# Kernel tuning notes

Hardware: AMD Instinct MI355X
Metric: run time of the kernel (lower is better)

The kernel has to match this reference:

```python
import jax, jax.numpy as jnp
import numpy as np

COMPRESSION = 2  # max-pool factor along flattened spatial axis for phi and g


def setup_inputs() -> dict:
    key = jax.random.key(0)
    ks = jax.random.split(key, 5)
    B, C, H, W = 4, 64, 96, 96
    Ci = 32  # intermediate_dim = C // 2
    s = 1.0 / np.sqrt(C)
    return {
        "x": jax.random.normal(ks[0], (B, C, H, W), dtype=jnp.float32),
        "w_theta": jax.random.normal(ks[1], (Ci, C), dtype=jnp.float32) * s,
        "b_theta": jnp.zeros((Ci,), dtype=jnp.float32),
        "w_phi": jax.random.normal(ks[2], (Ci, C), dtype=jnp.float32) * s,
        "b_phi": jnp.zeros((Ci,), dtype=jnp.float32),
        "w_g": jax.random.normal(ks[3], (Ci, C), dtype=jnp.float32) * s,
        "b_g": jnp.zeros((Ci,), dtype=jnp.float32),
        "w_out": jax.random.normal(ks[4], (C, Ci), dtype=jnp.float32) * (1.0 / np.sqrt(Ci)),
        "b_out": jnp.zeros((C,), dtype=jnp.float32),
    }


def reference(x, w_theta, b_theta, w_phi, b_phi, w_g, b_g, w_out, b_out):
    B, C, H, W = x.shape
    N = H * W
    xf = x.reshape(B, C, N).transpose(0, 2, 1)            # [B, N, C]
    # 1x1 conv projections == channel matmuls
    theta = xf @ w_theta.T + b_theta                      # [B, N, Ci]
    phi = xf @ w_phi.T + b_phi                            # [B, N, Ci]
    g = xf @ w_g.T + b_g                                  # [B, N, Ci]
    # compression: max-pool (kernel=stride=COMPRESSION) along flattened spatial axis
    Ci = theta.shape[-1]
    phi = phi.reshape(B, N // COMPRESSION, COMPRESSION, Ci).max(axis=2)  # [B, N/c, Ci]
    g = g.reshape(B, N // COMPRESSION, COMPRESSION, Ci).max(axis=2)      # [B, N/c, Ci]
    # embedded-gaussian affinity + softmax
    attn = jax.nn.softmax(jnp.einsum('bnc,bmc->bnm', theta, phi), axis=-1)  # [B, N, N/c]
    y = jnp.einsum('bnm,bmc->bnc', attn, g)               # [B, N, Ci]
    out = y @ w_out.T + b_out                             # [B, N, C]
    out = out.transpose(0, 2, 1).reshape(B, C, H, W)
    return out + x  # residual
```

## Files before the change

### kernel.cpp

```cpp
#include <hip/hip_runtime.h>
#include <hip/hip_bf16.h>


#define NQ 9216
#define MM 4608
#define TPW 36
#define LOG2E 1.44269504088896340736f

typedef __attribute__((ext_vector_type(8))) short bf16x8;
typedef __attribute__((ext_vector_type(4))) float f32x4;
typedef __attribute__((ext_vector_type(4))) unsigned short u16x4;

static __device__ __forceinline__ unsigned pk2(float a, float b) {
    __hip_bfloat162 h = __float22bfloat162_rn(make_float2(a, b));
    return *reinterpret_cast<unsigned*>(&h);
}

__global__ __launch_bounds__(128, 4) void proj_kernel(
    const float* __restrict__ x,
    const float* __restrict__ wt, const float* __restrict__ bt,
    const float* __restrict__ wp, const float* __restrict__ bp,
    const float* __restrict__ wg, const float* __restrict__ bg,
    unsigned short* __restrict__ theta, unsigned short* __restrict__ phi,
    unsigned short* __restrict__ gT)
{
    __shared__ unsigned short gst[32 * 20];

    const int tid  = threadIdx.x;
    const int wid  = tid >> 6;
    const int lane = tid & 63;
    const int q = lane >> 4;
    const int c = lane & 15;

    const int b     = blockIdx.x / 288;
    const int rem   = blockIdx.x % 288;
    const int n0    = rem * 32 + wid * 16;

    const float* Wm[3] = {wt, wp, wg};
    const float* Bm[3] = {bt, bp, bg};

    bf16x8 wf[3][2][2];
    float bias[3][2];
#pragma unroll
    for (int p = 0; p < 3; ++p) {
#pragma unroll
        for (int ct = 0; ct < 2; ++ct) {
            bias[p][ct] = Bm[p][ct * 16 + c];
#pragma unroll
            for (int ks = 0; ks < 2; ++ks) {
                const float* wsrc = Wm[p] + (ct * 16 + c) * 64 + ks * 32 + q * 8;
                f32x4 w0 = *(const f32x4*)wsrc;
                f32x4 w1 = *(const f32x4*)(wsrc + 4);
                unsigned* wk = (unsigned*)&wf[p][ct][ks];
                wk[0] = pk2(w0[0], w0[1]); wk[1] = pk2(w0[2], w0[3]);
                wk[2] = pk2(w1[0], w1[1]); wk[3] = pk2(w1[2], w1[3]);
            }
        }
    }

    bf16x8 af[2];
#pragma unroll
    for (int ks = 0; ks < 2; ++ks) {
        unsigned* ap = (unsigned*)&af[ks];
#pragma unroll
        for (int j2 = 0; j2 < 4; ++j2) {
            float x0 = x[(b * 64 + ks * 32 + q * 8 + j2 * 2) * NQ + n0 + c];
            float x1 = x[(b * 64 + ks * 32 + q * 8 + j2 * 2 + 1) * NQ + n0 + c];
            ap[j2] = pk2(x0, x1);
        }
    }

#pragma unroll
    for (int p = 0; p < 3; ++p) {
#pragma unroll
        for (int ct = 0; ct < 2; ++ct) {
            f32x4 acc = {0.f, 0.f, 0.f, 0.f};
            acc = __builtin_amdgcn_mfma_f32_16x16x32_bf16(af[0], wf[p][ct][0], acc, 0, 0, 0);
            acc = __builtin_amdgcn_mfma_f32_16x16x32_bf16(af[1], wf[p][ct][1], acc, 0, 0, 0);
#pragma unroll
            for (int r = 0; r < 4; ++r) acc[r] += bias[p][ct];
            const int ci = ct * 16 + c;
            if (p == 0) {
                unsigned pv0 = pk2(acc[0] * LOG2E, acc[1] * LOG2E);
                unsigned pv1 = pk2(acc[2] * LOG2E, acc[3] * LOG2E);
                theta[(b * NQ + n0 + 4 * q + 0) * 32 + ci] = (unsigned short)pv0;
                theta[(b * NQ + n0 + 4 * q + 1) * 32 + ci] = (unsigned short)(pv0 >> 16);
                theta[(b * NQ + n0 + 4 * q + 2) * 32 + ci] = (unsigned short)pv1;
                theta[(b * NQ + n0 + 4 * q + 3) * 32 + ci] = (unsigned short)(pv1 >> 16);
            } else {
                unsigned pv = pk2(fmaxf(acc[0], acc[1]), fmaxf(acc[2], acc[3]));
                if (p == 1) {
                    const int m0 = (n0 >> 1) + 2 * q;
                    phi[(b * MM + m0) * 32 + ci]     = (unsigned short)pv;
                    phi[(b * MM + m0 + 1) * 32 + ci] = (unsigned short)(pv >> 16);
                } else {
                    *(unsigned int*)(gst + ci * 20 + wid * 8 + 2 * q) = pv;
                }
            }
        }
    }

    __syncthreads();
    {
        const int ci = tid >> 2;
        const int m4 = (tid & 3) * 4;
        u16x4 v = *(const u16x4*)(gst + ci * 20 + m4);
        *(u16x4*)(gT + (b * 32 + ci) * MM + rem * 16 + m4) = v;
    }
}

__global__ __launch_bounds__(256, 4) void attn_kernel(
    const unsigned short* __restrict__ theta, const unsigned short* __restrict__ phi,
    const unsigned short* __restrict__ gT,
    const float* __restrict__ w_out, const float* __restrict__ b_out,
    const float* __restrict__ x, float* __restrict__ out)
{
    __shared__ union SharedU {
        unsigned short pld[4][48 * 32];
        struct {
            float red[4][48][36];
            float lred[4][48];
            unsigned short yld[32][50];
        } ep;
    } sh;

    const int tid  = threadIdx.x;
    const int w    = tid >> 6;
    const int lane = tid & 63;
    const int q  = lane >> 4;
    const int c  = lane & 15;
    const int sw = ((c >> 1) & 3) << 3;

    const int b  = blockIdx.x / 192;
    const int nb = (blockIdx.x % 192) * 48;

    bf16x8 qf[3];
#pragma unroll
    for (int rt = 0; rt < 3; ++rt)
        qf[rt] = *(const bf16x8*)(theta + (b * NQ + nb + rt * 16 + c) * 32 + q * 8);

    const unsigned short* phiB = phi + (size_t)b * MM * 32;
    const unsigned short* gTB  = gT + (size_t)b * 32 * MM;
    unsigned short* myp = sh.pld[w];

    f32x4 acc[3][2];
    float lsum[3];
#pragma unroll
    for (int rt = 0; rt < 3; ++rt) {
        lsum[rt] = 0.f;
#pragma unroll
        for (int s2 = 0; s2 < 2; ++s2) acc[rt][s2] = (f32x4){0.f, 0.f, 0.f, 0.f};
    }

    const int t0 = w * TPW;
    bf16x8 kf[2], vf[2];

#define LOAD_KF(m0) do {                                                      \
    kf[0] = *(const bf16x8*)(phiB + ((m0) + c) * 32 + q * 8);                 \
    kf[1] = *(const bf16x8*)(phiB + ((m0) + 16 + c) * 32 + q * 8);            \
} while (0)

#define LOAD_VF(m0) do {                                                      \
    vf[0] = *(const bf16x8*)(gTB + c * MM + (m0) + q * 8);                    \
    vf[1] = *(const bf16x8*)(gTB + (16 + c) * MM + (m0) + q * 8);             \
} while (0)

#define S_STEP(rt) do {                                                      \
    _Pragma("unroll")                                                        \
    for (int mct = 0; mct < 2; ++mct) {                                      \
        f32x4 z = {0.f, 0.f, 0.f, 0.f};                                      \
        f32x4 s = __builtin_amdgcn_mfma_f32_16x16x32_bf16(kf[mct], qf[rt], z, 0, 0, 0); \
        float e0 = __builtin_amdgcn_exp2f(s[0]);                             \
        float e1 = __builtin_amdgcn_exp2f(s[1]);                             \
        float e2 = __builtin_amdgcn_exp2f(s[2]);                             \
        float e3 = __builtin_amdgcn_exp2f(s[3]);                             \
        lsum[rt] += (e0 + e1) + (e2 + e3);                                   \
        uint2 hv = {pk2(e0, e1), pk2(e2, e3)};                               \
        *(uint2*)(myp + (((rt) * 16 + c) << 5) + ((mct * 16 + 4 * q) ^ sw)) = hv; \
    }                                                                        \
} while (0)

#define PV_STEP(rt) do {                                                     \
    bf16x8 pf = *(const bf16x8*)(myp + (((rt) * 16 + c) << 5) + ((q * 8) ^ sw)); \
    acc[rt][0] = __builtin_amdgcn_mfma_f32_16x16x32_bf16(vf[0], pf, acc[rt][0], 0, 0, 0); \
    acc[rt][1] = __builtin_amdgcn_mfma_f32_16x16x32_bf16(vf[1], pf, acc[rt][1], 0, 0, 0); \
} while (0)

    LOAD_KF(t0 * 32);
    LOAD_VF(t0 * 32);
    S_STEP(0); S_STEP(1); S_STEP(2);

    for (int mi = 1; mi < TPW; ++mi) {
        const int m0 = (t0 + mi) * 32;
        LOAD_KF(m0);
        PV_STEP(0); PV_STEP(1); PV_STEP(2);
        LOAD_VF(m0);
        S_STEP(0); S_STEP(1); S_STEP(2);
    }

    PV_STEP(0); PV_STEP(1); PV_STEP(2);

#undef LOAD_KF
#undef LOAD_VF
#undef S_STEP
#undef PV_STEP

    float lv[3];
#pragma unroll
    for (int rt = 0; rt < 3; ++rt) {
        float v = lsum[rt];
        v += __shfl_xor(v, 16);
        v += __shfl_xor(v, 32);
        lv[rt] = v;
    }

    __syncthreads();

    if (lane < 16) {
        sh.ep.lred[w][lane]      = lv[0];
        sh.ep.lred[w][16 + lane] = lv[1];
        sh.ep.lred[w][32 + lane] = lv[2];
    }
#pragma unroll
    for (int rt = 0; rt < 3; ++rt)
#pragma unroll
        for (int s2 = 0; s2 < 2; ++s2)
            *(f32x4*)&sh.ep.red[w][rt * 16 + c][s2 * 16 + 4 * q] = acc[rt][s2];

    __syncthreads();

    if (tid < 192) {
        const int n   = tid % 48;
        const int cig = (tid / 48) * 8;
        float ls = (sh.ep.lred[0][n] + sh.ep.lred[1][n]) +
                   (sh.ep.lred[2][n] + sh.ep.lred[3][n]);
        float inv = 1.0f / ls;
        f32x4 s0 = {0.f, 0.f, 0.f, 0.f}, s1 = {0.f, 0.f, 0.f, 0.f};
#pragma unroll
        for (int ww = 0; ww < 4; ++ww) {
            s0 += *(const f32x4*)&sh.ep.red[ww][n][cig];
            s1 += *(const f32x4*)&sh.ep.red[ww][n][cig + 4];
        }
#pragma unroll
        for (int k = 0; k < 4; ++k) {
            sh.ep.yld[cig + k][n]     = (unsigned short)(pk2(s0[k] * inv, 0.f) & 0xffff);
            sh.ep.yld[cig + 4 + k][n] = (unsigned short)(pk2(s1[k] * inv, 0.f) & 0xffff);
        }
    }
    __syncthreads();

    {
        bf16x8 wof;
        {
            const float* wsrc = w_out + (w * 16 + c) * 32 + q * 8;
            f32x4 w0 = *(const f32x4*)wsrc;
            f32x4 w1 = *(const f32x4*)(wsrc + 4);
            unsigned* wk = (unsigned*)&wof;
            wk[0] = pk2(w0[0], w0[1]); wk[1] = pk2(w0[2], w0[3]);
            wk[2] = pk2(w1[0], w1[1]); wk[3] = pk2(w1[2], w1[3]);
        }
#pragma unroll
        for (int nt = 0; nt < 3; ++nt) {
            bf16x8 yf;
            unsigned short* yp = (unsigned short*)&yf;
#pragma unroll
            for (int j = 0; j < 8; ++j)
                yp[j] = sh.ep.yld[q * 8 + j][nt * 16 + c];
            f32x4 z = {0.f, 0.f, 0.f, 0.f};
            f32x4 o = __builtin_amdgcn_mfma_f32_16x16x32_bf16(wof, yf, z, 0, 0, 0);
#pragma unroll
            for (int r = 0; r < 4; ++r) {
                const int chn = w * 16 + 4 * q + r;
                const size_t addr = (size_t)(b * 64 + chn) * NQ + nb + nt * 16 + c;
                out[addr] = o[r] + b_out[chn] + x[addr];
            }
        }
    }
}

extern "C" void kernel_launch(void* const* d_in, const int* in_sizes, int n_in,
                              void* d_out, int out_size, void* d_ws, size_t ws_size,
                              hipStream_t stream) {
    const float* x       = (const float*)d_in[0];
    const float* w_theta = (const float*)d_in[1];
    const float* b_theta = (const float*)d_in[2];
    const float* w_phi   = (const float*)d_in[3];
    const float* b_phi   = (const float*)d_in[4];
    const float* w_g     = (const float*)d_in[5];
    const float* b_g     = (const float*)d_in[6];
    const float* w_out   = (const float*)d_in[7];
    const float* b_out   = (const float*)d_in[8];
    float* out = (float*)d_out;

    unsigned short* theta = (unsigned short*)d_ws;
    unsigned short* phi   = theta + 4 * NQ * 32;
    unsigned short* gT    = phi + 4 * MM * 32;

    proj_kernel<<<1152, 128, 0, stream>>>(x, w_theta, b_theta, w_phi, b_phi,
                                          w_g, b_g, theta, phi, gT);
    attn_kernel<<<768, 256, 0, stream>>>(theta, phi, gT, w_out, b_out, x, out);
}
```

Measured before the change: 129.4 us.

## Compute softmax row sums with an MFMA and double proj work per block

The attention kernel no longer accumulates the softmax denominator with scalar adds and cross-lane shuffles. It runs an extra MFMA per PV step against a ones-vector operand, so the row sums come out of the matrix unit and take the bf16-rounded probabilities as input. This moves VALU work onto the matrix pipe but adds one MFMA for every two existing ones. Separately, the projection kernel now handles 64 spatial positions per block instead of 32, halving the grid and amortizing the weight loads and conversion, with a larger shared staging tile for the transposed g.

```diff
diff --git a/kernel.cpp b/kernel.cpp
--- a/kernel.cpp
+++ b/kernel.cpp
@@ -24,7 +24,7 @@
     unsigned short* __restrict__ theta, unsigned short* __restrict__ phi,
     unsigned short* __restrict__ gT)
 {
-    __shared__ unsigned short gst[32 * 20];
+    __shared__ unsigned short gst[32 * 36];
 
     const int tid  = threadIdx.x;
     const int wid  = tid >> 6;
@@ -32,9 +32,9 @@
     const int q = lane >> 4;
     const int c = lane & 15;
 
-    const int b     = blockIdx.x / 288;
-    const int rem   = blockIdx.x % 288;
-    const int n0    = rem * 32 + wid * 16;
+    const int b   = blockIdx.x / 144;
+    const int rem = blockIdx.x % 144;
+    const int n0  = rem * 64 + wid * 32;
 
     const float* Wm[3] = {wt, wp, wg};
     const float* Bm[3] = {bt, bp, bg};
@@ -58,43 +58,48 @@
         }
     }
 
-    bf16x8 af[2];
-#pragma unroll
-    for (int ks = 0; ks < 2; ++ks) {
-        unsigned* ap = (unsigned*)&af[ks];
-#pragma unroll
-        for (int j2 = 0; j2 < 4; ++j2) {
-            float x0 = x[(b * 64 + ks * 32 + q * 8 + j2 * 2) * NQ + n0 + c];
-            float x1 = x[(b * 64 + ks * 32 + q * 8 + j2 * 2 + 1) * NQ + n0 + c];
-            ap[j2] = pk2(x0, x1);
-        }
-    }
-
-#pragma unroll
-    for (int p = 0; p < 3; ++p) {
-#pragma unroll
-        for (int ct = 0; ct < 2; ++ct) {
-            f32x4 acc = {0.f, 0.f, 0.f, 0.f};
-            acc = __builtin_amdgcn_mfma_f32_16x16x32_bf16(af[0], wf[p][ct][0], acc, 0, 0, 0);
-            acc = __builtin_amdgcn_mfma_f32_16x16x32_bf16(af[1], wf[p][ct][1], acc, 0, 0, 0);
-#pragma unroll
-            for (int r = 0; r < 4; ++r) acc[r] += bias[p][ct];
-            const int ci = ct * 16 + c;
-            if (p == 0) {
-                unsigned pv0 = pk2(acc[0] * LOG2E, acc[1] * LOG2E);
-                unsigned pv1 = pk2(acc[2] * LOG2E, acc[3] * LOG2E);
-                theta[(b * NQ + n0 + 4 * q + 0) * 32 + ci] = (unsigned short)pv0;
-                theta[(b * NQ + n0 + 4 * q + 1) * 32 + ci] = (unsigned short)(pv0 >> 16);
-                theta[(b * NQ + n0 + 4 * q + 2) * 32 + ci] = (unsigned short)pv1;
-                theta[(b * NQ + n0 + 4 * q + 3) * 32 + ci] = (unsigned short)(pv1 >> 16);
-            } else {
-                unsigned pv = pk2(fmaxf(acc[0], acc[1]), fmaxf(acc[2], acc[3]));
-                if (p == 1) {
-                    const int m0 = (n0 >> 1) + 2 * q;
-                    phi[(b * MM + m0) * 32 + ci]     = (unsigned short)pv;
-                    phi[(b * MM + m0 + 1) * 32 + ci] = (unsigned short)(pv >> 16);
+#pragma unroll
+    for (int nt = 0; nt < 2; ++nt) {
+        const int n0t = n0 + nt * 16;
+
+        bf16x8 af[2];
+#pragma unroll
+        for (int ks = 0; ks < 2; ++ks) {
+            unsigned* ap = (unsigned*)&af[ks];
+#pragma unroll
+            for (int j2 = 0; j2 < 4; ++j2) {
+                float x0 = x[(b * 64 + ks * 32 + q * 8 + j2 * 2) * NQ + n0t + c];
+                float x1 = x[(b * 64 + ks * 32 + q * 8 + j2 * 2 + 1) * NQ + n0t + c];
+                ap[j2] = pk2(x0, x1);
+            }
+        }
+
+#pragma unroll
+        for (int p = 0; p < 3; ++p) {
+#pragma unroll
+            for (int ct = 0; ct < 2; ++ct) {
+                f32x4 acc = {0.f, 0.f, 0.f, 0.f};
+                acc = __builtin_amdgcn_mfma_f32_16x16x32_bf16(af[0], wf[p][ct][0], acc, 0, 0, 0);
+                acc = __builtin_amdgcn_mfma_f32_16x16x32_bf16(af[1], wf[p][ct][1], acc, 0, 0, 0);
+#pragma unroll
+                for (int r = 0; r < 4; ++r) acc[r] += bias[p][ct];
+                const int ci = ct * 16 + c;
+                if (p == 0) {
+                    unsigned pv0 = pk2(acc[0] * LOG2E, acc[1] * LOG2E);
+                    unsigned pv1 = pk2(acc[2] * LOG2E, acc[3] * LOG2E);
+                    theta[(b * NQ + n0t + 4 * q + 0) * 32 + ci] = (unsigned short)pv0;
+                    theta[(b * NQ + n0t + 4 * q + 1) * 32 + ci] = (unsigned short)(pv0 >> 16);
+                    theta[(b * NQ + n0t + 4 * q + 2) * 32 + ci] = (unsigned short)pv1;
+                    theta[(b * NQ + n0t + 4 * q + 3) * 32 + ci] = (unsigned short)(pv1 >> 16);
                 } else {
-                    *(unsigned int*)(gst + ci * 20 + wid * 8 + 2 * q) = pv;
+                    unsigned pv = pk2(fmaxf(acc[0], acc[1]), fmaxf(acc[2], acc[3]));
+                    if (p == 1) {
+                        const int m0 = (n0t >> 1) + 2 * q;
+                        phi[(b * MM + m0) * 32 + ci]     = (unsigned short)pv;
+                        phi[(b * MM + m0 + 1) * 32 + ci] = (unsigned short)(pv >> 16);
+                    } else {
+                        *(unsigned int*)(gst + ci * 36 + wid * 16 + nt * 8 + 2 * q) = pv;
+                    }
                 }
             }
         }
@@ -103,9 +108,12 @@
     __syncthreads();
     {
         const int ci = tid >> 2;
-        const int m4 = (tid & 3) * 4;
-        u16x4 v = *(const u16x4*)(gst + ci * 20 + m4);
-        *(u16x4*)(gT + (b * 32 + ci) * MM + rem * 16 + m4) = v;
+        const int m8 = (tid & 3) * 8;
+        u16x4 v0 = *(const u16x4*)(gst + ci * 36 + m8);
+        u16x4 v1 = *(const u16x4*)(gst + ci * 36 + m8 + 4);
+        unsigned short* dst = gT + (size_t)(b * 32 + ci) * MM + rem * 32 + m8;
+        *(u16x4*)dst       = v0;
+        *(u16x4*)(dst + 4) = v1;
     }
 }
 
@@ -139,15 +147,22 @@
     for (int rt = 0; rt < 3; ++rt)
         qf[rt] = *(const bf16x8*)(theta + (b * NQ + nb + rt * 16 + c) * 32 + q * 8);
 
+    bf16x8 onef;
+    {
+        unsigned v = (c == 0) ? 0x3F803F80u : 0u;
+        unsigned* op = (unsigned*)&onef;
+        op[0] = v; op[1] = v; op[2] = v; op[3] = v;
+    }
+
     const unsigned short* phiB = phi + (size_t)b * MM * 32;
     const unsigned short* gTB  = gT + (size_t)b * 32 * MM;
     unsigned short* myp = sh.pld[w];
 
     f32x4 acc[3][2];
-    float lsum[3];
+    f32x4 lacc[3];
 #pragma unroll
     for (int rt = 0; rt < 3; ++rt) {
-        lsum[rt] = 0.f;
+        lacc[rt] = (f32x4){0.f, 0.f, 0.f, 0.f};
 #pragma unroll
         for (int s2 = 0; s2 < 2; ++s2) acc[rt][s2] = (f32x4){0.f, 0.f, 0.f, 0.f};
     }
@@ -170,13 +185,9 @@
     for (int mct = 0; mct < 2; ++mct) {                                      \
         f32x4 z = {0.f, 0.f, 0.f, 0.f};                                      \
         f32x4 s = __builtin_amdgcn_mfma_f32_16x16x32_bf16(kf[mct], qf[rt], z, 0, 0, 0); \
-        float e0 = __builtin_amdgcn_exp2f(s[0]);                             \
-        float e1 = __builtin_amdgcn_exp2f(s[1]);                             \
-        float e2 = __builtin_amdgcn_exp2f(s[2]);                             \
-        float e3 = __builtin_amdgcn_exp2f(s[3]);                             \
-        lsum[rt] += (e0 + e1) + (e2 + e3);                                   \
-        uint2 hv = {pk2(e0, e1), pk2(e2, e3)};                               \
-        *(uint2*)(myp + (((rt) * 16 + c) << 5) + ((mct * 16 + 4 * q) ^ sw)) = hv; \
+        uint2 hv = {pk2(__builtin_amdgcn_exp2f(s[0]), __builtin_amdgcn_exp2f(s[1])),    \
+                    pk2(__builtin_amdgcn_exp2f(s[2]), __builtin_amdgcn_exp2f(s[3]))};   \
+        *(uint2*)(myp + (((rt) * 16 + c) << 5) + ((mct * 16 + 4 * q) ^ sw)) = hv;       \
     }                                                                        \
 } while (0)
 
@@ -184,6 +195,7 @@
     bf16x8 pf = *(const bf16x8*)(myp + (((rt) * 16 + c) << 5) + ((q * 8) ^ sw)); \
     acc[rt][0] = __builtin_amdgcn_mfma_f32_16x16x32_bf16(vf[0], pf, acc[rt][0], 0, 0, 0); \
     acc[rt][1] = __builtin_amdgcn_mfma_f32_16x16x32_bf16(vf[1], pf, acc[rt][1], 0, 0, 0); \
+    lacc[rt]   = __builtin_amdgcn_mfma_f32_16x16x32_bf16(onef,  pf, lacc[rt],   0, 0, 0); \
 } while (0)
 
     LOAD_KF(t0 * 32);
@@ -205,21 +217,12 @@
 #undef S_STEP
 #undef PV_STEP
 
-    float lv[3];
-#pragma unroll
-    for (int rt = 0; rt < 3; ++rt) {
-        float v = lsum[rt];
-        v += __shfl_xor(v, 16);
-        v += __shfl_xor(v, 32);
-        lv[rt] = v;
-    }
-
     __syncthreads();
 
     if (lane < 16) {
-        sh.ep.lred[w][lane]      = lv[0];
-        sh.ep.lred[w][16 + lane] = lv[1];
-        sh.ep.lred[w][32 + lane] = lv[2];
+        sh.ep.lred[w][lane]      = lacc[0][0];
+        sh.ep.lred[w][16 + lane] = lacc[1][0];
+        sh.ep.lred[w][32 + lane] = lacc[2][0];
     }
 #pragma unroll
     for (int rt = 0; rt < 3; ++rt)
@@ -296,7 +299,7 @@
     unsigned short* phi   = theta + 4 * NQ * 32;
     unsigned short* gT    = phi + 4 * MM * 32;
 
-    proj_kernel<<<1152, 128, 0, stream>>>(x, w_theta, b_theta, w_phi, b_phi,
-                                          w_g, b_g, theta, phi, gT);
+    proj_kernel<<<576, 128, 0, stream>>>(x, w_theta, b_theta, w_phi, b_phi,
+                                         w_g, b_g, theta, phi, gT);
     attn_kernel<<<768, 256, 0, stream>>>(theta, phi, gT, w_out, b_out, x, out);
 }
```

Result: faster. 125.5 us, median of 2 (-3.0%).
